# Optimization experiments

Measured on AMD Instinct MI355X. Metric: run time of the kernel, lower is better.

The kernel has to match this reference:

```python
import jax, jax.numpy as jnp
import numpy as np

B = 65536
L_IN = 1024
DS_FACTOR = 4  # 1024 -> 256 per DownsampleLY so cat gives 512


def fwht(x):
    """Fast Walsh-Hadamard transform over last dim, orthonormal (1/sqrt(n)) scaling."""
    n = x.shape[-1]
    lead = x.shape[:-1]
    h = 1
    while h < n:
        xr = x.reshape(lead + (n // (2 * h), 2, h))
        a = xr[..., 0, :]
        b = xr[..., 1, :]
        x = jnp.stack((a + b, a - b), axis=-2).reshape(lead + (n,))
        h *= 2
    return x * jnp.asarray(1.0 / np.sqrt(n), x.dtype)


def setup_inputs() -> dict:
    key = jax.random.key(0)
    ks = jax.random.split(key, 20)
    s = 0.05  # small init scale for numerical stability
    inp = {
        "x": jax.random.normal(ks[0], (B, L_IN), jnp.float32),
        # learnable downsample taps (factor-4 weighted pooling)
        "dw1": jax.random.normal(ks[1], (DS_FACTOR,), jnp.float32) * 0.25 + 0.25,
        "dw2": jax.random.normal(ks[2], (DS_FACTOR,), jnp.float32) * 0.25 + 0.25,
        # encoder: 512->512->128->64
        "eW1": jax.random.normal(ks[3], (512, 512), jnp.float32) * s,
        "eb1": jnp.zeros((512,), jnp.float32),
        "eW2": jax.random.normal(ks[4], (512, 128), jnp.float32) * s,
        "eb2": jnp.zeros((128,), jnp.float32),
        "eW3": jax.random.normal(ks[5], (128, 64), jnp.float32) * s,
        "eb3": jnp.zeros((64,), jnp.float32),
        # WHT1D channel mix (in=out=1 -> scalar scale + bias)
        "w1c": jnp.ones((), jnp.float32),
        "w1b": jnp.zeros((), jnp.float32),
        # decoder: 64->128->32
        "dW1": jax.random.normal(ks[6], (64, 128), jnp.float32) * s,
        "db1": jnp.zeros((128,), jnp.float32),
        "dW2": jax.random.normal(ks[7], (128, 32), jnp.float32) * s,
        "db2": jnp.zeros((32,), jnp.float32),
        "w2c": jnp.ones((), jnp.float32),
        "w2b": jnp.zeros((), jnp.float32),
        # proj: 32->32
        "pW": jax.random.normal(ks[8], (32, 32), jnp.float32) * s,
        "pb": jnp.zeros((32,), jnp.float32),
    }
    return inp


def reference(x, dw1, dw2, eW1, eb1, eW2, eb2, eW3, eb3, w1c, w1b,
              dW1, db1, dW2, db2, w2c, w2b, pW, pb):
    b = x.shape[0]
    xr = x.reshape(b, L_IN // DS_FACTOR, DS_FACTOR)  # (B, 256, 4)
    R = jnp.einsum('btk,k->bt', xr, dw1)             # (B, 256)
    Z = jnp.einsum('btk,k->bt', xr, dw2)             # (B, 256)
    h = jnp.concatenate((R, Z), axis=1)              # (B, 512)
    # encoder MLP
    h = jax.nn.relu(h @ eW1 + eb1)
    h = jax.nn.relu(h @ eW2 + eb2)
    h = h @ eW3 + eb3                                # (B, 64)
    # WHT1D(64) with 1x1 channel mix
    h = fwht(h) * w1c + w1b
    # decoder MLP
    h = jax.nn.relu(h @ dW1 + db1)
    h = h @ dW2 + db2                                # (B, 32)
    # WHT1D(32)
    h = fwht(h) * w2c + w2b
    # final projection -> (B, 32): [:,:16] real, [:,16:] imag
    return h @ pW + pb
```

## Files before the change

kernel.cpp:

```cpp
#include <hip/hip_runtime.h>

typedef _Float16 f16x8 __attribute__((ext_vector_type(8)));
typedef float f32x4 __attribute__((ext_vector_type(4)));

#define MFMA16(a, b, c) __builtin_amdgcn_mfma_f32_16x16x32_f16(a, b, c, 0, 0, 0)

#define OFF_W1   0u
#define OFF_W2   524288u
#define OFF_W3   655360u
#define OFF_W4   671744u
#define OFF_W5   688128u
#define OFF_W6   696320u
#define OFF_DB1  698368u
#define OFF_PB   698880u

__device__ inline void packw(int local, int N, const float* __restrict__ W,
                             _Float16* __restrict__ dst) {
  int j = local & 7;
  int lane = (local >> 3) & 63;
  int fi = local >> 9;
  int NF = N >> 4;
  int nf = fi % NF;
  int kk = fi / NF;
  int k = kk * 32 + ((lane >> 4) << 3) + j;
  int n = (nf << 4) + (lane & 15);
  dst[local] = (_Float16)W[k * N + n];
}

__device__ inline void packh(int local, int N, int K, const float* __restrict__ W,
                             _Float16* __restrict__ dst, float scale) {
  int j = local & 7;
  int lane = (local >> 3) & 63;
  int fi = local >> 9;
  int NF = N >> 4;
  int nf = fi % NF;
  int kk = fi / NF;
  int k = kk * 32 + ((lane >> 4) << 3) + j;
  int n = (nf << 4) + (lane & 15);
  float s = 0.f;
  for (int m = 0; m < K; ++m) {
    float v = W[m * N + n];
    s += (__popc(k & m) & 1) ? -v : v;
  }
  dst[local] = (_Float16)(s * scale);
}

extern "C" __global__ __launch_bounds__(256) void prep_kernel(
    const float* __restrict__ eW1, const float* __restrict__ eW2,
    const float* __restrict__ eW3, const float* __restrict__ dW1,
    const float* __restrict__ dW2, const float* __restrict__ pW,
    const float* __restrict__ w1c, const float* __restrict__ w1b,
    const float* __restrict__ w2c, const float* __restrict__ w2b,
    const float* __restrict__ db1, const float* __restrict__ pb,
    char* __restrict__ ws) {
  int idx = blockIdx.x * 256 + threadIdx.x;
  if (idx < 262144) {
    packw(idx, 512, eW1, (_Float16*)(ws + OFF_W1));
  } else if (idx < 327680) {
    packw(idx - 262144, 128, eW2, (_Float16*)(ws + OFF_W2));
  } else if (idx < 335872) {
    packw(idx - 327680, 64, eW3, (_Float16*)(ws + OFF_W3));
  } else if (idx < 344064) {
    packh(idx - 335872, 128, 64, dW1, (_Float16*)(ws + OFF_W4), w1c[0] * 0.125f);
  } else if (idx < 348160) {
    packw(idx - 344064, 32, dW2, (_Float16*)(ws + OFF_W5));
  } else if (idx < 349184) {
    packh(idx - 348160, 32, 32, pW, (_Float16*)(ws + OFF_W6),
          w2c[0] * 0.17677669529663687f);
  } else if (idx < 349312) {
    int n = idx - 349184;
    float s = 0.f;
    for (int m = 0; m < 64; ++m) s += dW1[m * 128 + n];
    ((float*)(ws + OFF_DB1))[n] = db1[n] + w1b[0] * s;
  } else if (idx < 349344) {
    int n = idx - 349312;
    float s = 0.f;
    for (int m = 0; m < 32; ++m) s += pW[m * 32 + n];
    ((float*)(ws + OFF_PB))[n] = pb[n] + w2b[0] * s;
  }
}

__device__ inline int hidx(int row, int col, int nu) {
  int u = (col >> 3) ^ ((row & 7) & (nu - 1));
  return row * (nu << 3) + (u << 3) + (col & 7);
}

__device__ inline f16x8 afrag(const _Float16* h, int row, int col, int nu) {
  return *(const f16x8*)(h + hidx(row, col, nu));
}

template <int KK, int NUIN, int NUOUT, bool RELU, int MT>
__device__ inline void layerN(const _Float16* hin, _Float16* hout,
                              const f16x8* __restrict__ Wp,
                              const float* __restrict__ bias, int NFtot, int m0,
                              int nf0, int lane, int g, int rr) {
  f32x4 acc[MT];
#pragma unroll
  for (int m = 0; m < MT; ++m) acc[m] = (f32x4){0.f, 0.f, 0.f, 0.f};
#pragma unroll
  for (int kk = 0; kk < KK; ++kk) {
    f16x8 b = Wp[(kk * NFtot + nf0) * 64 + lane];
#pragma unroll
    for (int m = 0; m < MT; ++m) {
      f16x8 a = afrag(hin, (m0 + m) * 16 + rr, kk * 32 + g * 8, NUIN);
      acc[m] = MFMA16(a, b, acc[m]);
    }
  }
  const int n = nf0 * 16 + rr;
  const float bv = bias[n];
#pragma unroll
  for (int m = 0; m < MT; ++m) {
#pragma unroll
    for (int i = 0; i < 4; ++i) {
      float v = acc[m][i] + bv;
      if (RELU) v = fmaxf(v, 0.f);
      hout[hidx((m0 + m) * 16 + g * 4 + i, n, NUOUT)] = (_Float16)v;
    }
  }
}

#define LDC(C)                                              \
  do {                                                      \
    const float4* p0_ = xrow0 + (C) * 32;                   \
    const float4* p1_ = xrow1 + (C) * 32;                   \
    q0 = p0_[e];  q1 = p0_[e + 8];  q2 = p0_[e + 16];  q3 = p0_[e + 24]; \
    q4 = p1_[e];  q5 = p1_[e + 8];  q6 = p1_[e + 16];  q7 = p1_[e + 24]; \
  } while (0)

#define DOTR(V) (_Float16)((V).x * d10 + (V).y * d11 + (V).z * d12 + (V).w * d13)
#define DOTZ(V) (_Float16)((V).x * d20 + (V).y * d21 + (V).z * d22 + (V).w * d23)

#define CONVQ(V, ROW, J)                                          \
  do {                                                            \
    int ix_ = (ROW) * 32 + ((((J) ^ ((ROW) & 3))) << 3) + e;      \
    sliceR[ix_] = DOTR(V);                                        \
    sliceZ[ix_] = DOTZ(V);                                        \
  } while (0)

#define CONVC                                                     \
  do {                                                            \
    CONVQ(q0, r8, 0); CONVQ(q1, r8, 1); CONVQ(q2, r8, 2); CONVQ(q3, r8, 3); \
    CONVQ(q4, r8 + 64, 0); CONVQ(q5, r8 + 64, 1); CONVQ(q6, r8 + 64, 2); CONVQ(q7, r8 + 64, 3); \
  } while (0)

#define GRID 512

extern "C" __global__ __launch_bounds__(512)
__attribute__((amdgpu_waves_per_eu(2, 2))) void fused_kernel(
    const float* __restrict__ x, const float* __restrict__ dw1,
    const float* __restrict__ dw2, const float* __restrict__ eb1,
    const float* __restrict__ eb2, const float* __restrict__ eb3,
    const float* __restrict__ db2, const char* __restrict__ ws,
    float* __restrict__ out) {
  __shared__ __align__(16) _Float16 LDS[73728];
  _Float16* const h1 = LDS;
  _Float16* const sliceR = LDS + 65536;
  _Float16* const sliceZ = LDS + 69632;
  _Float16* const h2 = LDS;
  _Float16* const h3 = LDS + 16384;
  _Float16* const h4 = LDS + 24576;
  _Float16* const h5 = LDS + 40960;

  const int tid = threadIdx.x;
  const int wg = blockIdx.x;
  const int lane = tid & 63;
  const int w = tid >> 6;
  const int g = lane >> 4;
  const int rr = lane & 15;
  const int r8 = tid >> 3;
  const int e = tid & 7;

  const float d10 = dw1[0], d11 = dw1[1], d12 = dw1[2], d13 = dw1[3];
  const float d20 = dw2[0], d21 = dw2[1], d22 = dw2[2], d23 = dw2[3];

  const f16x8* __restrict__ W1 = (const f16x8*)(ws + OFF_W1);
  const f16x8* __restrict__ W2 = (const f16x8*)(ws + OFF_W2);
  const f16x8* __restrict__ W3 = (const f16x8*)(ws + OFF_W3);
  const f16x8* __restrict__ W4 = (const f16x8*)(ws + OFF_W4);
  const f16x8* __restrict__ W5 = (const f16x8*)(ws + OFF_W5);
  const f16x8* __restrict__ W6 = (const f16x8*)(ws + OFF_W6);
  const float* __restrict__ db1p = (const float*)(ws + OFF_DB1);
  const float* __restrict__ pbp = (const float*)(ws + OFF_PB);

  const float4* __restrict__ xrow0 =
      (const float4*)x + ((size_t)wg * 128 + r8) * 256;
  const float4* __restrict__ xrow1 = xrow0 + (size_t)64 * 256;

  float4 q0, q1, q2, q3, q4, q5, q6, q7;

  LDC(0);
  CONVC;
  __syncthreads();

  f32x4 acc[8][4];
#pragma unroll
  for (int m = 0; m < 8; ++m)
#pragma unroll
    for (int n = 0; n < 4; ++n) acc[m][n] = (f32x4){0.f, 0.f, 0.f, 0.f};

  for (int c = 0; c < 8; ++c) {
    if (c < 7) LDC(c + 1);
#pragma unroll
    for (int S = 0; S < 2; ++S) {
      const _Float16* sl = S ? sliceZ : sliceR;
      const int kk = S ? (8 + c) : c;
      f16x8 a0 = afrag(sl, rr, g * 8, 4);
      f16x8 a1 = afrag(sl, 16 + rr, g * 8, 4);
      f16x8 a2 = afrag(sl, 32 + rr, g * 8, 4);
      f16x8 a3 = afrag(sl, 48 + rr, g * 8, 4);
      f16x8 a4 = afrag(sl, 64 + rr, g * 8, 4);
      f16x8 a5 = afrag(sl, 80 + rr, g * 8, 4);
      f16x8 a6 = afrag(sl, 96 + rr, g * 8, 4);
      f16x8 a7 = afrag(sl, 112 + rr, g * 8, 4);
#pragma unroll
      for (int nf = 0; nf < 4; ++nf) {
        f16x8 b = W1[(kk * 32 + w * 4 + nf) * 64 + lane];
        acc[0][nf] = MFMA16(a0, b, acc[0][nf]);
        acc[1][nf] = MFMA16(a1, b, acc[1][nf]);
        acc[2][nf] = MFMA16(a2, b, acc[2][nf]);
        acc[3][nf] = MFMA16(a3, b, acc[3][nf]);
        acc[4][nf] = MFMA16(a4, b, acc[4][nf]);
        acc[5][nf] = MFMA16(a5, b, acc[5][nf]);
        acc[6][nf] = MFMA16(a6, b, acc[6][nf]);
        acc[7][nf] = MFMA16(a7, b, acc[7][nf]);
      }
    }
    if (c < 7) {
      __syncthreads();
      CONVC;
      __syncthreads();
    }
  }

#pragma unroll
  for (int mt = 0; mt < 8; ++mt) {
#pragma unroll
    for (int nf = 0; nf < 4; ++nf) {
      const int n = (w * 4 + nf) * 16 + rr;
      const float bv = eb1[n];
#pragma unroll
      for (int i = 0; i < 4; ++i) {
        float v = fmaxf(acc[mt][nf][i] + bv, 0.f);
        h1[hidx(mt * 16 + g * 4 + i, n, 64)] = (_Float16)v;
      }
    }
  }
  __syncthreads();

  layerN<16, 64, 16, true, 8>(h1, h2, W2, eb2, 8, 0, w, lane, g, rr);
  __syncthreads();
  layerN<4, 16, 8, false, 4>(h2, h3, W3, eb3, 4, (w >> 2) * 4, w & 3, lane, g, rr);
  __syncthreads();
  layerN<2, 8, 16, true, 8>(h3, h4, W4, db1p, 8, 0, w, lane, g, rr);
  __syncthreads();
  layerN<4, 16, 4, false, 2>(h4, h5, W5, db2, 2, (w >> 1) * 2, w & 1, lane, g, rr);
  __syncthreads();

  {
    const int m0 = (w >> 1) * 2;
    const int nf0 = w & 1;
    const int n = nf0 * 16 + rr;
    const float bv = pbp[n];
#pragma unroll
    for (int m = 0; m < 2; ++m) {
      f16x8 a = afrag(h5, (m0 + m) * 16 + rr, g * 8, 4);
      f16x8 b = W6[nf0 * 64 + lane];
      f32x4 o = MFMA16(a, b, ((f32x4){0.f, 0.f, 0.f, 0.f}));
      const size_t rbase = (size_t)wg * 128 + (m0 + m) * 16;
#pragma unroll
      for (int i = 0; i < 4; ++i) {
        out[(rbase + g * 4 + i) * 32 + n] = o[i] + bv;
      }
    }
  }
}

extern "C" void kernel_launch(void* const* d_in, const int* in_sizes, int n_in,
                              void* d_out, int out_size, void* d_ws, size_t ws_size,
                              hipStream_t stream) {
  const float* x = (const float*)d_in[0];
  const float* dw1 = (const float*)d_in[1];
  const float* dw2 = (const float*)d_in[2];
  const float* eW1 = (const float*)d_in[3];
  const float* eb1 = (const float*)d_in[4];
  const float* eW2 = (const float*)d_in[5];
  const float* eb2 = (const float*)d_in[6];
  const float* eW3 = (const float*)d_in[7];
  const float* eb3 = (const float*)d_in[8];
  const float* w1c = (const float*)d_in[9];
  const float* w1b = (const float*)d_in[10];
  const float* dW1 = (const float*)d_in[11];
  const float* db1 = (const float*)d_in[12];
  const float* dW2 = (const float*)d_in[13];
  const float* db2 = (const float*)d_in[14];
  const float* w2c = (const float*)d_in[15];
  const float* w2b = (const float*)d_in[16];
  const float* pW = (const float*)d_in[17];
  const float* pb = (const float*)d_in[18];
  char* ws = (char*)d_ws;
  float* out = (float*)d_out;

  prep_kernel<<<dim3(1365), dim3(256), 0, stream>>>(eW1, eW2, eW3, dW1, dW2, pW, w1c, w1b,
                                                    w2c, w2b, db1, pb, ws);
  fused_kernel<<<dim3(GRID), dim3(512), 0, stream>>>(x, dw1, dw2, eb1, eb2, eb3, db2, ws,
                                                     out);
}
```

Before: 84.01 us.

## Persist workgroups over two row blocks and prefetch next block's first chunk into LDS

```diff
diff --git a/kernel.cpp b/kernel.cpp
--- a/kernel.cpp
+++ b/kernel.cpp
@@ -89,36 +89,6 @@
   return *(const f16x8*)(h + hidx(row, col, nu));
 }
 
-template <int KK, int NUIN, int NUOUT, bool RELU, int MT>
-__device__ inline void layerN(const _Float16* hin, _Float16* hout,
-                              const f16x8* __restrict__ Wp,
-                              const float* __restrict__ bias, int NFtot, int m0,
-                              int nf0, int lane, int g, int rr) {
-  f32x4 acc[MT];
-#pragma unroll
-  for (int m = 0; m < MT; ++m) acc[m] = (f32x4){0.f, 0.f, 0.f, 0.f};
-#pragma unroll
-  for (int kk = 0; kk < KK; ++kk) {
-    f16x8 b = Wp[(kk * NFtot + nf0) * 64 + lane];
-#pragma unroll
-    for (int m = 0; m < MT; ++m) {
-      f16x8 a = afrag(hin, (m0 + m) * 16 + rr, kk * 32 + g * 8, NUIN);
-      acc[m] = MFMA16(a, b, acc[m]);
-    }
-  }
-  const int n = nf0 * 16 + rr;
-  const float bv = bias[n];
-#pragma unroll
-  for (int m = 0; m < MT; ++m) {
-#pragma unroll
-    for (int i = 0; i < 4; ++i) {
-      float v = acc[m][i] + bv;
-      if (RELU) v = fmaxf(v, 0.f);
-      hout[hidx((m0 + m) * 16 + g * 4 + i, n, NUOUT)] = (_Float16)v;
-    }
-  }
-}
-
 #define LDC(C)                                              \
   do {                                                      \
     const float4* p0_ = xrow0 + (C) * 32;                   \
@@ -130,20 +100,25 @@
 #define DOTR(V) (_Float16)((V).x * d10 + (V).y * d11 + (V).z * d12 + (V).w * d13)
 #define DOTZ(V) (_Float16)((V).x * d20 + (V).y * d21 + (V).z * d22 + (V).w * d23)
 
-#define CONVQ(V, ROW, J)                                          \
+#define CONVQ2(V, ROW, JJ, EL)                                    \
   do {                                                            \
-    int ix_ = (ROW) * 32 + ((((J) ^ ((ROW) & 3))) << 3) + e;      \
+    int ix_ = (ROW) * 32 + ((((JJ) ^ ((ROW) & 3))) << 3) + (EL);  \
     sliceR[ix_] = DOTR(V);                                        \
     sliceZ[ix_] = DOTZ(V);                                        \
   } while (0)
 
 #define CONVC                                                     \
   do {                                                            \
-    CONVQ(q0, r8, 0); CONVQ(q1, r8, 1); CONVQ(q2, r8, 2); CONVQ(q3, r8, 3); \
-    CONVQ(q4, r8 + 64, 0); CONVQ(q5, r8 + 64, 1); CONVQ(q6, r8 + 64, 2); CONVQ(q7, r8 + 64, 3); \
+    CONVQ2(q0, r8, 0, e); CONVQ2(q1, r8, 1, e);                   \
+    CONVQ2(q2, r8, 2, e); CONVQ2(q3, r8, 3, e);                   \
+    CONVQ2(q4, r8 + 64, 0, e); CONVQ2(q5, r8 + 64, 1, e);         \
+    CONVQ2(q6, r8 + 64, 2, e); CONVQ2(q7, r8 + 64, 3, e);         \
   } while (0)
 
-#define GRID 512
+#define RAWBAR asm volatile("s_waitcnt lgkmcnt(0)\n\ts_barrier" ::: "memory")
+
+#define NB 2
+#define GRID 256
 
 extern "C" __global__ __launch_bounds__(512)
 __attribute__((amdgpu_waves_per_eu(2, 2))) void fused_kernel(
@@ -154,12 +129,12 @@
     float* __restrict__ out) {
   __shared__ __align__(16) _Float16 LDS[73728];
   _Float16* const h1 = LDS;
+  _Float16* const h2 = LDS;
+  _Float16* const h4 = LDS + 16384;
+  _Float16* const h5 = LDS;
+  _Float16* const h3 = LDS + 65536;
   _Float16* const sliceR = LDS + 65536;
   _Float16* const sliceZ = LDS + 69632;
-  _Float16* const h2 = LDS;
-  _Float16* const h3 = LDS + 16384;
-  _Float16* const h4 = LDS + 24576;
-  _Float16* const h5 = LDS + 40960;
 
   const int tid = threadIdx.x;
   const int wg = blockIdx.x;
@@ -182,94 +157,220 @@
   const float* __restrict__ db1p = (const float*)(ws + OFF_DB1);
   const float* __restrict__ pbp = (const float*)(ws + OFF_PB);
 
-  const float4* __restrict__ xrow0 =
-      (const float4*)x + ((size_t)wg * 128 + r8) * 256;
-  const float4* __restrict__ xrow1 = xrow0 + (size_t)64 * 256;
-
   float4 q0, q1, q2, q3, q4, q5, q6, q7;
 
-  LDC(0);
-  CONVC;
-  __syncthreads();
-
-  f32x4 acc[8][4];
-#pragma unroll
-  for (int m = 0; m < 8; ++m)
-#pragma unroll
-    for (int n = 0; n < 4; ++n) acc[m][n] = (f32x4){0.f, 0.f, 0.f, 0.f};
-
-  for (int c = 0; c < 8; ++c) {
-    if (c < 7) LDC(c + 1);
-#pragma unroll
-    for (int S = 0; S < 2; ++S) {
-      const _Float16* sl = S ? sliceZ : sliceR;
-      const int kk = S ? (8 + c) : c;
-      f16x8 a0 = afrag(sl, rr, g * 8, 4);
-      f16x8 a1 = afrag(sl, 16 + rr, g * 8, 4);
-      f16x8 a2 = afrag(sl, 32 + rr, g * 8, 4);
-      f16x8 a3 = afrag(sl, 48 + rr, g * 8, 4);
-      f16x8 a4 = afrag(sl, 64 + rr, g * 8, 4);
-      f16x8 a5 = afrag(sl, 80 + rr, g * 8, 4);
-      f16x8 a6 = afrag(sl, 96 + rr, g * 8, 4);
-      f16x8 a7 = afrag(sl, 112 + rr, g * 8, 4);
-#pragma unroll
-      for (int nf = 0; nf < 4; ++nf) {
-        f16x8 b = W1[(kk * 32 + w * 4 + nf) * 64 + lane];
-        acc[0][nf] = MFMA16(a0, b, acc[0][nf]);
-        acc[1][nf] = MFMA16(a1, b, acc[1][nf]);
-        acc[2][nf] = MFMA16(a2, b, acc[2][nf]);
-        acc[3][nf] = MFMA16(a3, b, acc[3][nf]);
-        acc[4][nf] = MFMA16(a4, b, acc[4][nf]);
-        acc[5][nf] = MFMA16(a5, b, acc[5][nf]);
-        acc[6][nf] = MFMA16(a6, b, acc[6][nf]);
-        acc[7][nf] = MFMA16(a7, b, acc[7][nf]);
-      }
-    }
-    if (c < 7) {
-      __syncthreads();
+  for (int b = 0; b < NB; ++b) {
+    const size_t blkIdx = (size_t)wg + (size_t)GRID * b;
+    const float4* __restrict__ xrow0 =
+        (const float4*)x + (blkIdx * 128 + r8) * 256;
+    const float4* __restrict__ xrow1 = xrow0 + (size_t)64 * 256;
+
+    if (b == 0) {
+      LDC(0);
       CONVC;
       __syncthreads();
-    }
-  }
-
-#pragma unroll
-  for (int mt = 0; mt < 8; ++mt) {
-#pragma unroll
-    for (int nf = 0; nf < 4; ++nf) {
-      const int n = (w * 4 + nf) * 16 + rr;
-      const float bv = eb1[n];
+    } else {
+      asm volatile("s_waitcnt vmcnt(0)" ::: "memory");
+      __syncthreads();
+      const float* rawf = (const float*)((const char*)LDS + 65536);
+      const int el = e ^ (r8 & 7);
+#pragma unroll
+      for (int jj = 0; jj < 4; ++jj) {
+        int colp = el + 8 * jj;
+        float4 v0 = *(const float4*)(rawf + r8 * 128 + colp * 4);
+        float4 v1 = *(const float4*)(rawf + (r8 + 64) * 128 + colp * 4);
+        CONVQ2(v0, r8, jj, el);
+        CONVQ2(v1, r8 + 64, jj, el);
+      }
+      __syncthreads();
+    }
+
+    f32x4 acc[8][4];
+#pragma unroll
+    for (int m = 0; m < 8; ++m)
+#pragma unroll
+      for (int n = 0; n < 4; ++n) acc[m][n] = (f32x4){0.f, 0.f, 0.f, 0.f};
+
+    for (int c = 0; c < 8; ++c) {
+      if (c < 7) LDC(c + 1);
+#pragma unroll
+      for (int S = 0; S < 2; ++S) {
+        const _Float16* sl = S ? sliceZ : sliceR;
+        const int kk = S ? (8 + c) : c;
+        f16x8 a0 = afrag(sl, rr, g * 8, 4);
+        f16x8 a1 = afrag(sl, 16 + rr, g * 8, 4);
+        f16x8 a2 = afrag(sl, 32 + rr, g * 8, 4);
+        f16x8 a3 = afrag(sl, 48 + rr, g * 8, 4);
+        f16x8 a4 = afrag(sl, 64 + rr, g * 8, 4);
+        f16x8 a5 = afrag(sl, 80 + rr, g * 8, 4);
+        f16x8 a6 = afrag(sl, 96 + rr, g * 8, 4);
+        f16x8 a7 = afrag(sl, 112 + rr, g * 8, 4);
+#pragma unroll
+        for (int nf = 0; nf < 4; ++nf) {
+          f16x8 bb = W1[(kk * 32 + w * 4 + nf) * 64 + lane];
+          acc[0][nf] = MFMA16(a0, bb, acc[0][nf]);
+          acc[1][nf] = MFMA16(a1, bb, acc[1][nf]);
+          acc[2][nf] = MFMA16(a2, bb, acc[2][nf]);
+          acc[3][nf] = MFMA16(a3, bb, acc[3][nf]);
+          acc[4][nf] = MFMA16(a4, bb, acc[4][nf]);
+          acc[5][nf] = MFMA16(a5, bb, acc[5][nf]);
+          acc[6][nf] = MFMA16(a6, bb, acc[6][nf]);
+          acc[7][nf] = MFMA16(a7, bb, acc[7][nf]);
+        }
+      }
+      if (c < 7) {
+        __syncthreads();
+        CONVC;
+        __syncthreads();
+      }
+    }
+
+#pragma unroll
+    for (int mt = 0; mt < 8; ++mt) {
+#pragma unroll
+      for (int nf = 0; nf < 4; ++nf) {
+        const int n = (w * 4 + nf) * 16 + rr;
+        const float bv = eb1[n];
+#pragma unroll
+        for (int i = 0; i < 4; ++i) {
+          float v = fmaxf(acc[mt][nf][i] + bv, 0.f);
+          h1[hidx(mt * 16 + g * 4 + i, n, 64)] = (_Float16)v;
+        }
+      }
+    }
+    __syncthreads();
+
+    f32x4 acc2[8];
+#pragma unroll
+    for (int m = 0; m < 8; ++m) acc2[m] = (f32x4){0.f, 0.f, 0.f, 0.f};
+#pragma unroll
+    for (int kk = 0; kk < 16; ++kk) {
+      f16x8 b2 = W2[(kk * 8 + w) * 64 + lane];
+#pragma unroll
+      for (int m = 0; m < 8; ++m) {
+        f16x8 a = afrag(h1, m * 16 + rr, kk * 32 + g * 8, 64);
+        acc2[m] = MFMA16(a, b2, acc2[m]);
+      }
+    }
+    const float bv2 = eb2[w * 16 + rr];
+    __syncthreads();
+
+    const int nf3 = w & 3, m3 = (w >> 2) * 4;
+    const int nf5 = w & 1, m5 = (w >> 1) * 2;
+    f16x8 b3f0 = W3[(0 * 4 + nf3) * 64 + lane];
+    f16x8 b3f1 = W3[(1 * 4 + nf3) * 64 + lane];
+    f16x8 b3f2 = W3[(2 * 4 + nf3) * 64 + lane];
+    f16x8 b3f3 = W3[(3 * 4 + nf3) * 64 + lane];
+    f16x8 b4f0 = W4[(0 * 8 + w) * 64 + lane];
+    f16x8 b4f1 = W4[(1 * 8 + w) * 64 + lane];
+    f16x8 b5f0 = W5[(0 * 2 + nf5) * 64 + lane];
+    f16x8 b5f1 = W5[(1 * 2 + nf5) * 64 + lane];
+    f16x8 b5f2 = W5[(2 * 2 + nf5) * 64 + lane];
+    f16x8 b5f3 = W5[(3 * 2 + nf5) * 64 + lane];
+    f16x8 b6f = W6[nf5 * 64 + lane];
+    const float bv3 = eb3[nf3 * 16 + rr];
+    const float bv4 = db1p[w * 16 + rr];
+    const float bv5 = db2[nf5 * 16 + rr];
+    const float bv6 = pbp[nf5 * 16 + rr];
+    __builtin_amdgcn_sched_barrier(0);
+
+    if (b + 1 < NB) {
+      const size_t xoff = ((size_t)wg + (size_t)GRID * (b + 1)) * 131072;
+#pragma unroll
+      for (int j = 0; j < 8; ++j) {
+        int ell0 = (w * 8 + j) * 1024;
+        int ell = ell0 + lane * 16;
+        int row = ell >> 9;
+        int win = ell & 511;
+        const float* gp = x + xoff + (size_t)row * 1024 + (win >> 2);
+        __builtin_amdgcn_global_load_lds(
+            (const __attribute__((address_space(1))) void*)gp,
+            (__attribute__((address_space(3))) void*)((char*)LDS + 65536 + ell0),
+            16, 0, 0);
+      }
+    }
+    __builtin_amdgcn_sched_barrier(0);
+
+#pragma unroll
+    for (int m = 0; m < 8; ++m) {
 #pragma unroll
       for (int i = 0; i < 4; ++i) {
-        float v = fmaxf(acc[mt][nf][i] + bv, 0.f);
-        h1[hidx(mt * 16 + g * 4 + i, n, 64)] = (_Float16)v;
-      }
-    }
-  }
-  __syncthreads();
-
-  layerN<16, 64, 16, true, 8>(h1, h2, W2, eb2, 8, 0, w, lane, g, rr);
-  __syncthreads();
-  layerN<4, 16, 8, false, 4>(h2, h3, W3, eb3, 4, (w >> 2) * 4, w & 3, lane, g, rr);
-  __syncthreads();
-  layerN<2, 8, 16, true, 8>(h3, h4, W4, db1p, 8, 0, w, lane, g, rr);
-  __syncthreads();
-  layerN<4, 16, 4, false, 2>(h4, h5, W5, db2, 2, (w >> 1) * 2, w & 1, lane, g, rr);
-  __syncthreads();
-
-  {
-    const int m0 = (w >> 1) * 2;
-    const int nf0 = w & 1;
-    const int n = nf0 * 16 + rr;
-    const float bv = pbp[n];
-#pragma unroll
-    for (int m = 0; m < 2; ++m) {
-      f16x8 a = afrag(h5, (m0 + m) * 16 + rr, g * 8, 4);
-      f16x8 b = W6[nf0 * 64 + lane];
-      f32x4 o = MFMA16(a, b, ((f32x4){0.f, 0.f, 0.f, 0.f}));
-      const size_t rbase = (size_t)wg * 128 + (m0 + m) * 16;
-#pragma unroll
-      for (int i = 0; i < 4; ++i) {
-        out[(rbase + g * 4 + i) * 32 + n] = o[i] + bv;
+        float v = fmaxf(acc2[m][i] + bv2, 0.f);
+        h2[hidx(m * 16 + g * 4 + i, w * 16 + rr, 16)] = (_Float16)v;
+      }
+    }
+    RAWBAR;
+
+    {
+      f32x4 a3c[4];
+#pragma unroll
+      for (int m = 0; m < 4; ++m) a3c[m] = (f32x4){0.f, 0.f, 0.f, 0.f};
+#pragma unroll
+      for (int m = 0; m < 4; ++m) {
+        a3c[m] = MFMA16(afrag(h2, (m3 + m) * 16 + rr, 0 * 32 + g * 8, 16), b3f0, a3c[m]);
+        a3c[m] = MFMA16(afrag(h2, (m3 + m) * 16 + rr, 1 * 32 + g * 8, 16), b3f1, a3c[m]);
+        a3c[m] = MFMA16(afrag(h2, (m3 + m) * 16 + rr, 2 * 32 + g * 8, 16), b3f2, a3c[m]);
+        a3c[m] = MFMA16(afrag(h2, (m3 + m) * 16 + rr, 3 * 32 + g * 8, 16), b3f3, a3c[m]);
+      }
+#pragma unroll
+      for (int m = 0; m < 4; ++m)
+#pragma unroll
+        for (int i = 0; i < 4; ++i)
+          h3[hidx((m3 + m) * 16 + g * 4 + i, nf3 * 16 + rr, 8)] =
+              (_Float16)(a3c[m][i] + bv3);
+    }
+    RAWBAR;
+
+    {
+      f32x4 a4c[8];
+#pragma unroll
+      for (int m = 0; m < 8; ++m) a4c[m] = (f32x4){0.f, 0.f, 0.f, 0.f};
+#pragma unroll
+      for (int m = 0; m < 8; ++m) {
+        a4c[m] = MFMA16(afrag(h3, m * 16 + rr, 0 * 32 + g * 8, 8), b4f0, a4c[m]);
+        a4c[m] = MFMA16(afrag(h3, m * 16 + rr, 1 * 32 + g * 8, 8), b4f1, a4c[m]);
+      }
+#pragma unroll
+      for (int m = 0; m < 8; ++m)
+#pragma unroll
+        for (int i = 0; i < 4; ++i) {
+          float v = fmaxf(a4c[m][i] + bv4, 0.f);
+          h4[hidx(m * 16 + g * 4 + i, w * 16 + rr, 16)] = (_Float16)v;
+        }
+    }
+    RAWBAR;
+
+    {
+      f32x4 a5c[2];
+#pragma unroll
+      for (int m = 0; m < 2; ++m) a5c[m] = (f32x4){0.f, 0.f, 0.f, 0.f};
+#pragma unroll
+      for (int m = 0; m < 2; ++m) {
+        a5c[m] = MFMA16(afrag(h4, (m5 + m) * 16 + rr, 0 * 32 + g * 8, 16), b5f0, a5c[m]);
+        a5c[m] = MFMA16(afrag(h4, (m5 + m) * 16 + rr, 1 * 32 + g * 8, 16), b5f1, a5c[m]);
+        a5c[m] = MFMA16(afrag(h4, (m5 + m) * 16 + rr, 2 * 32 + g * 8, 16), b5f2, a5c[m]);
+        a5c[m] = MFMA16(afrag(h4, (m5 + m) * 16 + rr, 3 * 32 + g * 8, 16), b5f3, a5c[m]);
+      }
+#pragma unroll
+      for (int m = 0; m < 2; ++m)
+#pragma unroll
+        for (int i = 0; i < 4; ++i)
+          h5[hidx((m5 + m) * 16 + g * 4 + i, nf5 * 16 + rr, 4)] =
+              (_Float16)(a5c[m][i] + bv5);
+    }
+    RAWBAR;
+
+    {
+#pragma unroll
+      for (int m = 0; m < 2; ++m) {
+        f16x8 a = afrag(h5, (m5 + m) * 16 + rr, g * 8, 4);
+        f32x4 o = MFMA16(a, b6f, ((f32x4){0.f, 0.f, 0.f, 0.f}));
+        const size_t rbase = blkIdx * 128 + (m5 + m) * 16;
+        const int n = nf5 * 16 + rr;
+#pragma unroll
+        for (int i = 0; i < 4; ++i) {
+          out[(rbase + g * 4 + i) * 32 + n] = o[i] + bv6;
+        }
       }
     }
   }
```

New measurement: 320.8 us. +281.8%, slower.

## Double-buffer downsample slices in LDS and inline layer-2 GEMM

Applied to the files above, without the earlier changes.

```diff
diff --git a/kernel.cpp b/kernel.cpp
--- a/kernel.cpp
+++ b/kernel.cpp
@@ -130,17 +130,19 @@
 #define DOTR(V) (_Float16)((V).x * d10 + (V).y * d11 + (V).z * d12 + (V).w * d13)
 #define DOTZ(V) (_Float16)((V).x * d20 + (V).y * d21 + (V).z * d22 + (V).w * d23)
 
-#define CONVQ(V, ROW, J)                                          \
+#define CONVQ2(V, ROW, JJ, SR, SZ)                                \
   do {                                                            \
-    int ix_ = (ROW) * 32 + ((((J) ^ ((ROW) & 3))) << 3) + e;      \
-    sliceR[ix_] = DOTR(V);                                        \
-    sliceZ[ix_] = DOTZ(V);                                        \
+    int ix_ = (ROW) * 32 + ((((JJ) ^ ((ROW) & 3))) << 3) + e;     \
+    (SR)[ix_] = DOTR(V);                                          \
+    (SZ)[ix_] = DOTZ(V);                                          \
   } while (0)
 
-#define CONVC                                                     \
+#define CONVC(SR, SZ)                                             \
   do {                                                            \
-    CONVQ(q0, r8, 0); CONVQ(q1, r8, 1); CONVQ(q2, r8, 2); CONVQ(q3, r8, 3); \
-    CONVQ(q4, r8 + 64, 0); CONVQ(q5, r8 + 64, 1); CONVQ(q6, r8 + 64, 2); CONVQ(q7, r8 + 64, 3); \
+    CONVQ2(q0, r8, 0, SR, SZ); CONVQ2(q1, r8, 1, SR, SZ);         \
+    CONVQ2(q2, r8, 2, SR, SZ); CONVQ2(q3, r8, 3, SR, SZ);         \
+    CONVQ2(q4, r8 + 64, 0, SR, SZ); CONVQ2(q5, r8 + 64, 1, SR, SZ); \
+    CONVQ2(q6, r8 + 64, 2, SR, SZ); CONVQ2(q7, r8 + 64, 3, SR, SZ); \
   } while (0)
 
 #define GRID 512
@@ -154,12 +156,14 @@
     float* __restrict__ out) {
   __shared__ __align__(16) _Float16 LDS[73728];
   _Float16* const h1 = LDS;
-  _Float16* const sliceR = LDS + 65536;
-  _Float16* const sliceZ = LDS + 69632;
   _Float16* const h2 = LDS;
-  _Float16* const h3 = LDS + 16384;
-  _Float16* const h4 = LDS + 24576;
+  _Float16* const h4 = LDS + 16384;
   _Float16* const h5 = LDS + 40960;
+  _Float16* const h3 = LDS + 65536;
+  _Float16* const s0R = LDS + 49152;
+  _Float16* const s0Z = LDS + 53248;
+  _Float16* const s1R = LDS + 57344;
+  _Float16* const s1Z = LDS + 61440;
 
   const int tid = threadIdx.x;
   const int wg = blockIdx.x;
@@ -189,7 +193,7 @@
   float4 q0, q1, q2, q3, q4, q5, q6, q7;
 
   LDC(0);
-  CONVC;
+  CONVC(s0R, s0Z);
   __syncthreads();
 
   f32x4 acc[8][4];
@@ -200,9 +204,11 @@
 
   for (int c = 0; c < 8; ++c) {
     if (c < 7) LDC(c + 1);
+    const _Float16* sRp = (c & 1) ? s1R : s0R;
+    const _Float16* sZp = (c & 1) ? s1Z : s0Z;
 #pragma unroll
     for (int S = 0; S < 2; ++S) {
-      const _Float16* sl = S ? sliceZ : sliceR;
+      const _Float16* sl = S ? sZp : sRp;
       const int kk = S ? (8 + c) : c;
       f16x8 a0 = afrag(sl, rr, g * 8, 4);
       f16x8 a1 = afrag(sl, 16 + rr, g * 8, 4);
@@ -214,22 +220,23 @@
       f16x8 a7 = afrag(sl, 112 + rr, g * 8, 4);
 #pragma unroll
       for (int nf = 0; nf < 4; ++nf) {
-        f16x8 b = W1[(kk * 32 + w * 4 + nf) * 64 + lane];
-        acc[0][nf] = MFMA16(a0, b, acc[0][nf]);
-        acc[1][nf] = MFMA16(a1, b, acc[1][nf]);
-        acc[2][nf] = MFMA16(a2, b, acc[2][nf]);
-        acc[3][nf] = MFMA16(a3, b, acc[3][nf]);
-        acc[4][nf] = MFMA16(a4, b, acc[4][nf]);
-        acc[5][nf] = MFMA16(a5, b, acc[5][nf]);
-        acc[6][nf] = MFMA16(a6, b, acc[6][nf]);
-        acc[7][nf] = MFMA16(a7, b, acc[7][nf]);
+        f16x8 bb = W1[(kk * 32 + w * 4 + nf) * 64 + lane];
+        acc[0][nf] = MFMA16(a0, bb, acc[0][nf]);
+        acc[1][nf] = MFMA16(a1, bb, acc[1][nf]);
+        acc[2][nf] = MFMA16(a2, bb, acc[2][nf]);
+        acc[3][nf] = MFMA16(a3, bb, acc[3][nf]);
+        acc[4][nf] = MFMA16(a4, bb, acc[4][nf]);
+        acc[5][nf] = MFMA16(a5, bb, acc[5][nf]);
+        acc[6][nf] = MFMA16(a6, bb, acc[6][nf]);
+        acc[7][nf] = MFMA16(a7, bb, acc[7][nf]);
       }
     }
     if (c < 7) {
-      __syncthreads();
-      CONVC;
-      __syncthreads();
-    }
+      _Float16* dR = (c & 1) ? s0R : s1R;
+      _Float16* dZ = (c & 1) ? s0Z : s1Z;
+      CONVC(dR, dZ);
+    }
+    __syncthreads();
   }
 
 #pragma unroll
@@ -247,8 +254,32 @@
   }
   __syncthreads();
 
-  layerN<16, 64, 16, true, 8>(h1, h2, W2, eb2, 8, 0, w, lane, g, rr);
-  __syncthreads();
+  {
+    f32x4 acc2[8];
+#pragma unroll
+    for (int m = 0; m < 8; ++m) acc2[m] = (f32x4){0.f, 0.f, 0.f, 0.f};
+#pragma unroll
+    for (int kk = 0; kk < 16; ++kk) {
+      f16x8 b2 = W2[(kk * 8 + w) * 64 + lane];
+#pragma unroll
+      for (int m = 0; m < 8; ++m) {
+        f16x8 a = afrag(h1, m * 16 + rr, kk * 32 + g * 8, 64);
+        acc2[m] = MFMA16(a, b2, acc2[m]);
+      }
+    }
+    const float bv2 = eb2[w * 16 + rr];
+    __syncthreads();
+#pragma unroll
+    for (int m = 0; m < 8; ++m) {
+#pragma unroll
+      for (int i = 0; i < 4; ++i) {
+        float v = fmaxf(acc2[m][i] + bv2, 0.f);
+        h2[hidx(m * 16 + g * 4 + i, w * 16 + rr, 16)] = (_Float16)v;
+      }
+    }
+  }
+  __syncthreads();
+
   layerN<4, 16, 8, false, 4>(h2, h3, W3, eb3, 4, (w >> 2) * 4, w & 3, lane, g, rr);
   __syncthreads();
   layerN<2, 8, 16, true, 8>(h3, h4, W4, db1p, 8, 0, w, lane, g, rr);
@@ -257,19 +288,19 @@
   __syncthreads();
 
   {
-    const int m0 = (w >> 1) * 2;
-    const int nf0 = w & 1;
-    const int n = nf0 * 16 + rr;
-    const float bv = pbp[n];
+    const int m5 = (w >> 1) * 2;
+    const int nf5 = w & 1;
+    const int n = nf5 * 16 + rr;
+    const float bv6 = pbp[n];
+    f16x8 b6 = W6[nf5 * 64 + lane];
 #pragma unroll
     for (int m = 0; m < 2; ++m) {
-      f16x8 a = afrag(h5, (m0 + m) * 16 + rr, g * 8, 4);
-      f16x8 b = W6[nf0 * 64 + lane];
-      f32x4 o = MFMA16(a, b, ((f32x4){0.f, 0.f, 0.f, 0.f}));
-      const size_t rbase = (size_t)wg * 128 + (m0 + m) * 16;
+      f16x8 a = afrag(h5, (m5 + m) * 16 + rr, g * 8, 4);
+      f32x4 o = MFMA16(a, b6, ((f32x4){0.f, 0.f, 0.f, 0.f}));
+      const size_t rbase = (size_t)wg * 128 + (m5 + m) * 16;
 #pragma unroll
       for (int i = 0; i < 4; ++i) {
-        out[(rbase + g * 4 + i) * 32 + n] = o[i] + bv;
+        out[(rbase + g * 4 + i) * 32 + n] = o[i] + bv6;
       }
     }
   }
```

Result: faster. 79.74 us, median of 2 (-5.1%).
